# Performance work log

Hardware: AMD Instinct MI355X
Metric: run time of the kernel (lower is better)

Reference implementation:

```python
import jax, jax.numpy as jnp
import numpy as np

N_NODES = 100000
N_EDGES = 1600000
IN_F = 64
OUT_F = 64
GRID_SIZE = 5
SPLINE_ORDER = 3
GRID_MIN, GRID_MAX = -1.0, 1.0
N_COEF = GRID_SIZE + SPLINE_ORDER  # 8 spline coefficients per (in,out)


def make_grid():
    # Extended knot grid, shape (IN_F, GRID_SIZE + 2*SPLINE_ORDER + 1)
    h = (GRID_MAX - GRID_MIN) / GRID_SIZE
    pts = jnp.arange(-SPLINE_ORDER, GRID_SIZE + SPLINE_ORDER + 1, dtype=jnp.float32) * h + GRID_MIN
    return jnp.tile(pts[None, :], (IN_F, 1))


def b_splines(x, grid):
    # x: (N, IN_F) -> bases: (N, IN_F, N_COEF) via Cox-de Boor recursion
    xe = x[..., None]
    bases = ((xe >= grid[:, :-1]) & (xe < grid[:, 1:])).astype(x.dtype)
    for j in range(1, SPLINE_ORDER + 1):
        left = (xe - grid[:, : -(j + 1)]) / (grid[:, j:-1] - grid[:, : -(j + 1)])
        right = (grid[:, j + 1:] - xe) / (grid[:, j + 1:] - grid[:, 1:-j])
        bases = left * bases[..., :-1] + right * bases[..., 1:]
    return bases


def kan_apply(x, base_w, spline_w, grid):
    # base path: silu(x) @ W_b^T ; spline path: flattened B-spline bases @ W_s^T
    base = jnp.matmul(jax.nn.silu(x), base_w.T)
    sp = b_splines(x, grid).reshape(x.shape[0], -1)          # (N, IN_F*N_COEF)
    spline = jnp.matmul(sp, spline_w.reshape(OUT_F, -1).T)    # (N, OUT_F)
    return base + spline


def setup_inputs() -> dict:
    key = jax.random.key(0)
    k1, k2, k3, k4, k5, k6 = jax.random.split(key, 6)
    x = jax.random.normal(k1, (N_NODES, IN_F), dtype=jnp.float32)
    edge_index = jax.random.randint(k2, (2, N_EDGES), 0, N_NODES, dtype=jnp.int32)
    s = 1.0 / np.sqrt(IN_F)
    base_w_layer = jax.random.normal(k3, (OUT_F, IN_F), dtype=jnp.float32) * s
    spline_w_layer = jax.random.normal(k4, (OUT_F, IN_F, N_COEF), dtype=jnp.float32) * 0.1 * s
    base_w_conv = jax.random.normal(k5, (OUT_F, IN_F), dtype=jnp.float32) * s
    spline_w_conv = jax.random.normal(k6, (OUT_F, IN_F, N_COEF), dtype=jnp.float32) * 0.1 * s
    return {
        "x": x,
        "base_w_layer": base_w_layer,
        "spline_w_layer": spline_w_layer,
        "base_w_conv": base_w_conv,
        "spline_w_conv": spline_w_conv,
        "edge_index": edge_index,
    }


def reference(x, base_w_layer, spline_w_layer, base_w_conv, spline_w_conv, edge_index):
    grid = make_grid()
    src, dst = edge_index[0], edge_index[1]
    # A_hat symmetric normalization: deg^{-1/2}[src] * deg^{-1/2}[dst]
    deg = jax.ops.segment_sum(jnp.ones(src.shape[0], x.dtype), dst, num_segments=N_NODES)
    dinv = jnp.where(deg > 0, jax.lax.rsqrt(jnp.maximum(deg, 1.0)), 0.0)
    coef = dinv[src] * dinv[dst]                              # (E,)
    msg = x[src] * coef[:, None]                              # (E, IN_F) gather
    agg = jax.ops.segment_sum(msg, dst, num_segments=N_NODES) # (N, IN_F) scatter-add
    # aggregate_first=True: KAN transform applied after aggregation
    h_layer = kan_apply(x, base_w_layer, spline_w_layer, grid)
    h_conv = kan_apply(agg, base_w_conv, spline_w_conv, grid)
    return h_layer + h_conv
```

## Files before the change

### kernel.cpp

```cpp
#include <hip/hip_runtime.h>
#include <math.h>

#define N_NODES 100000
#define N_EDGES 1600000
#define IN_F 64
#define OUT_F 64

#define K_SLOT 10
#define CH_IF 16
#define AST 172
#define AGH 33
#define NB 64
#define NTHR 256
#define EMAXW 448

#define NBUCK 256
#define NBUCK_USED 196
#define BSH 9
#define BCAP 9728
#define BUCK_N 512
#define EPT 8
#define EPB 2048

#define NODES_PAD 100352
#define WF_U16 (8 * 20 * 512)
#define WG_SLOTS (WF_U16 / 2)
#define CSR_CAP (NBUCK_USED * BCAP)
#define OFF_DINV 0
#define OFF_ROWPTR (OFF_DINV + NODES_PAD)
#define OFF_ROWEND (OFF_ROWPTR + NODES_PAD)
#define OFF_WT (OFF_ROWEND + NODES_PAD)
#define OFF_BF (OFF_WT + WG_SLOTS)
#define OFF_CSR (OFF_BF + 256)
#define FIXED_SLOTS (OFF_CSR + CSR_CAP)
#define XH_SLOTS (N_NODES * IN_F / 2)
#define OFF_XH FIXED_SLOTS
#define FIXED2 (FIXED_SLOTS + XH_SLOTS)
#define AGG_ELEMS (N_NODES * IN_F)

typedef __attribute__((ext_vector_type(8))) short bf16x8;
typedef __attribute__((ext_vector_type(4))) short bf16x4;
typedef __attribute__((ext_vector_type(4))) float f32x4;

__device__ __forceinline__ unsigned int bf16_rne(float v) {
    unsigned int u = __float_as_uint(v);
    u += 0x7FFFu + ((u >> 16) & 1u);
    return u >> 16;
}

__global__ __launch_bounds__(256)
void bucket_bin_kernel(const int* __restrict__ ei, int* __restrict__ bf,
                       int2* __restrict__ pairs,
                       const float* __restrict__ x, unsigned short* __restrict__ xh) {
    __shared__ int lh[NBUCK];
    __shared__ int lbase[NBUCK];
    int t = threadIdx.x;
    lh[t] = 0;
    __syncthreads();
    int e0 = blockIdx.x * EPB;
    int d[EPT], s[EPT], lp[EPT];
#pragma unroll
    for (int k = 0; k < EPT; ++k) {
        int e = e0 + k * 256 + t;
        bool ok = e < N_EDGES;
        d[k] = ok ? ei[N_EDGES + e] : -1;
        s[k] = ok ? ei[e] : 0;
        lp[k] = ok ? atomicAdd(&lh[d[k] >> BSH], 1) : 0;
    }
    __syncthreads();
    if (lh[t]) {
        int r = atomicAdd(&bf[t], lh[t]);
        int cap = (t + 1) * BCAP - lh[t];
        lbase[t] = r > cap ? cap : r;
    }
    __syncthreads();
#pragma unroll
    for (int k = 0; k < EPT; ++k) {
        if (d[k] >= 0) {
            int b = d[k] >> BSH;
            pairs[lbase[b] + lp[k]] = make_int2(d[k], s[k]);
        }
    }
    int total = gridDim.x * 256;
    for (int i = blockIdx.x * 256 + t; i * 4 < N_NODES * IN_F; i += total) {
        float4 v = *(const float4*)&x[i * 4];
        uint2 u;
        u.x = bf16_rne(v.x) | (bf16_rne(v.y) << 16);
        u.y = bf16_rne(v.z) | (bf16_rne(v.w) << 16);
        *(uint2*)&xh[i * 4] = u;
    }
}

__global__ __launch_bounds__(BUCK_N)
void bucket_build_kernel(const int2* __restrict__ pairs, const int* __restrict__ bf,
                         int* __restrict__ rowptr, int* __restrict__ rowend,
                         float* __restrict__ dinv, int* __restrict__ csr) {
    __shared__ int ldeg[BUCK_N];
    __shared__ int sb[BUCK_N];
    __shared__ int lpos[BUCK_N];
    int t = threadIdx.x;
    int b = blockIdx.x;
    int base = b * BCAP;
    int cnt = bf[b] - base;
    if (cnt > BCAP) cnt = BCAP;
    ldeg[t] = 0;
    __syncthreads();
    for (int j = t; j < cnt; j += BUCK_N) atomicAdd(&ldeg[pairs[base + j].x & (BUCK_N - 1)], 1);
    __syncthreads();
    int v = ldeg[t];
    sb[t] = v;
    __syncthreads();
    for (int off = 1; off < BUCK_N; off <<= 1) {
        int add = (t >= off) ? sb[t - off] : 0;
        __syncthreads();
        sb[t] += add;
        __syncthreads();
    }
    int excl = sb[t] - v;
    int node = (b << BSH) + t;
    if (node < N_NODES) {
        rowptr[node] = base + excl;
        rowend[node] = base + excl + v;
        dinv[node] = (v > 0) ? rsqrtf((float)v) : 0.0f;
    }
    lpos[t] = base + excl;
    __syncthreads();
    for (int j = t; j < cnt; j += BUCK_N) {
        int2 p = pairs[base + j];
        int pos = atomicAdd(&lpos[p.x & (BUCK_N - 1)], 1);
        csr[pos] = p.y;
    }
}

__global__ __launch_bounds__(256)
void gather_kernel(const float* __restrict__ x, const int* __restrict__ csr,
                   const int* __restrict__ rowptr, const int* __restrict__ rowend,
                   const float* __restrict__ dinv, float* __restrict__ agg) {
    int wid = (int)((blockIdx.x * 256 + threadIdx.x) >> 6);
    int lane = threadIdx.x & 63;
    if (wid >= N_NODES) return;
    int start = rowptr[wid];
    int end = rowend[wid];
    float acc = 0.0f;
    int j = start;
    for (; j + 3 < end; j += 4) {
        int s0 = csr[j], s1 = csr[j + 1], s2 = csr[j + 2], s3 = csr[j + 3];
        float a0 = x[s0 * 64 + lane] * dinv[s0];
        float a1 = x[s1 * 64 + lane] * dinv[s1];
        float a2 = x[s2 * 64 + lane] * dinv[s2];
        float a3 = x[s3 * 64 + lane] * dinv[s3];
        acc += a0 + a1 + a2 + a3;
    }
    for (; j < end; ++j) {
        int s = csr[j];
        acc += x[s * 64 + lane] * dinv[s];
    }
    agg[wid * 64 + lane] = acc * dinv[wid];
}

__global__ void deg_kernel(const int* __restrict__ ei, float* __restrict__ deg) {
    int e = blockIdx.x * blockDim.x + threadIdx.x;
    if (e < N_EDGES) atomicAdd(&deg[ei[N_EDGES + e]], 1.0f);
}
__global__ void dinv_kernel(float* __restrict__ deg) {
    int n = blockIdx.x * blockDim.x + threadIdx.x;
    if (n < N_NODES) {
        float d = deg[n];
        deg[n] = (d > 0.0f) ? rsqrtf(d) : 0.0f;
    }
}
__global__ void scatter_kernel(const float* __restrict__ x, const int* __restrict__ ei,
                               const float* __restrict__ dinv, float* __restrict__ agg) {
    long long gtid = (long long)blockIdx.x * blockDim.x + threadIdx.x;
    int wid = (int)(gtid >> 6);
    int lane = threadIdx.x & 63;
    if (wid >= N_EDGES) return;
    int s = ei[wid];
    int d = ei[N_EDGES + wid];
    float c = dinv[s] * dinv[d];
    atomicAdd(&agg[d * 64 + lane], x[s * 64 + lane] * c);
}

__global__ void wprep_kernel(const float* __restrict__ bwl, const float* __restrict__ swl,
                             const float* __restrict__ bwc, const float* __restrict__ swc,
                             unsigned short* __restrict__ Wf, int* __restrict__ bf) {
    int gid = blockIdx.x * blockDim.x + threadIdx.x;
    if (bf && gid < NBUCK) bf[gid] = gid * BCAP;
    if (gid >= WF_U16) return;
    int fr = gid >> 9;
    int lj = gid & 511;
    int lane = lj >> 3, j = lj & 7;
    int ch = fr / 20, r2 = fr - ch * 20;
    int s = r2 >> 2, t = r2 & 3;
    int o = t * 16 + (lane & 15);
    int kk = ((lane >> 4) << 3) + s * 32 + j;
    int iL = kk / K_SLOT, c = kk - iL * K_SLOT;
    int i = (ch & 3) * CH_IF + iL;
    int path = ch >> 2;
    const float* bw = path ? bwc : bwl;
    const float* sw = path ? swc : swl;
    float v = 0.0f;
    if (c == 8) v = bw[o * IN_F + i];
    else if (c < 8) v = sw[o * 512 + i * 8 + c];
    Wf[gid] = (unsigned short)bf16_rne(v);
}

__device__ __forceinline__ void write_feat(unsigned short* Arow, int iL, float v) {
    unsigned int* Au = (unsigned int*)(Arow + iL * K_SLOT);
    float sig = __builtin_amdgcn_rcpf(1.0f + __expf(-v));
    Au[0] = 0u; Au[1] = 0u; Au[2] = 0u; Au[3] = 0u;
    Au[4] = bf16_rne(v * sig);
    float s5 = (v + 2.2f) * 2.5f;
    float fm = floorf(s5);
    int m = (int)fm;
    if (m >= 0 && m <= 10) {
        float t = s5 - fm;
        float omt = 1.0f - t;
        float t2 = t * t, t3 = t2 * t;
        float n0 = omt * omt * omt * (1.0f / 6.0f);
        float n3 = t3 * (1.0f / 6.0f);
        float n1 = 0.66666666f - t2 + 0.5f * t3;
        float n2 = 1.0f - n0 - n1 - n3;
        unsigned short* As = Arow + iL * K_SLOT;
        if (m >= 3)           As[m - 3] = (unsigned short)bf16_rne(n0);
        if (m >= 2 && m <= 9) As[m - 2] = (unsigned short)bf16_rne(n1);
        if (m >= 1 && m <= 8) As[m - 1] = (unsigned short)bf16_rne(n2);
        if (m <= 7)           As[m]     = (unsigned short)bf16_rne(n3);
    }
}

__global__ __launch_bounds__(NTHR, 4)
void kan_fused_kernel(const float* __restrict__ x, const unsigned short* __restrict__ xh,
                      const int* __restrict__ csr, const int* __restrict__ rowptr,
                      const int* __restrict__ rowend, const float* __restrict__ dinv,
                      const unsigned short* __restrict__ Wf, float* __restrict__ out) {
    __shared__ __align__(16) unsigned short A_lds[NB * AST];
    __shared__ unsigned int agg_lds[NB * AGH];
    __shared__ int csr_lds[4 * EMAXW];

    int tid = threadIdx.x;
    int nbase = blockIdx.x * NB;
    int wid = tid >> 6;
    int lane = tid & 63;
    int nloc0 = (wid << 4) + (lane & 15);
    int q = lane >> 4;
    int node0 = nbase + nloc0;
    bool ok0 = node0 < N_NODES;

    const float4 z4 = make_float4(0.f, 0.f, 0.f, 0.f);
    float4 vx[4];
#pragma unroll
    for (int c = 0; c < 4; ++c)
        vx[c] = ok0 ? *(const float4*)&x[node0 * 64 + c * CH_IF + q * 4] : z4;

    int wn0 = nbase + (wid << 4);
    int s0w = 0, slenw = 0;
    int* wcsr = &csr_lds[wid * EMAXW];
    if (wn0 < N_NODES) {
        int wnL = wn0 + 15;
        if (wnL >= N_NODES) wnL = N_NODES - 1;
        s0w = rowptr[wn0];
        slenw = rowend[wnL] - s0w;
        int cap = slenw < EMAXW ? slenw : EMAXW;
        for (int i = lane; i < cap; i += 64) wcsr[i] = csr[s0w + i];
    }

    f32x4 acc[4];
#pragma unroll
    for (int t = 0; t < 4; ++t) acc[t] = (f32x4){0.f, 0.f, 0.f, 0.f};

    int kfrag = (lane >> 4) * 8;
    const unsigned short* Abase = &A_lds[nloc0 * AST + kfrag];
    unsigned short* Arow = &A_lds[nloc0 * AST];
    const bf16x8* Bbase = (const bf16x8*)Wf + lane;

    auto do_chunk = [&](int chunk) {
        float vv[4];
        if (chunk < 4) {
            vv[0] = vx[chunk].x; vv[1] = vx[chunk].y; vv[2] = vx[chunk].z; vv[3] = vx[chunk].w;
        } else {
            int b2 = (chunk - 4) * 8 + q * 2;
            unsigned u0 = agg_lds[nloc0 * AGH + b2];
            unsigned u1 = agg_lds[nloc0 * AGH + b2 + 1];
            vv[0] = __uint_as_float(u0 << 16);
            vv[1] = __uint_as_float(u0 & 0xFFFF0000u);
            vv[2] = __uint_as_float(u1 << 16);
            vv[3] = __uint_as_float(u1 & 0xFFFF0000u);
        }
#pragma unroll
        for (int jj = 0; jj < 4; ++jj) write_feat(Arow, q * 4 + jj, vv[jj]);
#pragma unroll
        for (int s = 0; s < 5; ++s) {
            bf16x4 alo = *(const bf16x4*)(Abase + s * 32);
            bf16x4 ahi = *(const bf16x4*)(Abase + s * 32 + 4);
            bf16x8 a = __builtin_shufflevector(alo, ahi, 0, 1, 2, 3, 4, 5, 6, 7);
#pragma unroll
            for (int t = 0; t < 4; ++t) {
                bf16x8 b = Bbase[((chunk * 5 + s) * 4 + t) * 64];
                acc[t] = __builtin_amdgcn_mfma_f32_16x16x32_bf16(a, b, acc[t], 0, 0, 0);
            }
        }
    };

    auto do_gather = [&]() {
        int half = lane >> 5;
        int l = lane & 31;
        const unsigned int* xh32 = (const unsigned int*)xh;
        for (int p = 0; p < 8; ++p) {
            int nloc = (wid << 4) + (p << 1) + half;
            int nd = nbase + nloc;
            float ax = 0.f, ay = 0.f, dn = 0.f;
            if (nd < N_NODES) {
                dn = dinv[nd];
                int j = rowptr[nd] - s0w;
                int end = rowend[nd] - s0w;
                if (end <= EMAXW) {
                    for (; j + 15 < end; j += 16) {
                        int sa[16]; unsigned ua[16]; float da[16];
#pragma unroll
                        for (int k = 0; k < 16; ++k) sa[k] = wcsr[j + k];
#pragma unroll
                        for (int k = 0; k < 16; ++k) ua[k] = xh32[sa[k] * 32 + l];
#pragma unroll
                        for (int k = 0; k < 16; ++k) da[k] = dinv[sa[k]];
#pragma unroll
                        for (int k = 0; k < 16; ++k) {
                            ax += __uint_as_float(ua[k] << 16) * da[k];
                            ay += __uint_as_float(ua[k] & 0xFFFF0000u) * da[k];
                        }
                    }
                    for (; j + 3 < end; j += 4) {
                        int s0 = wcsr[j], s1 = wcsr[j + 1], s2 = wcsr[j + 2], s3 = wcsr[j + 3];
                        unsigned u0 = xh32[s0 * 32 + l], u1 = xh32[s1 * 32 + l];
                        unsigned u2 = xh32[s2 * 32 + l], u3 = xh32[s3 * 32 + l];
                        float d0 = dinv[s0], d1 = dinv[s1], d2 = dinv[s2], d3 = dinv[s3];
                        ax += __uint_as_float(u0 << 16) * d0 + __uint_as_float(u1 << 16) * d1
                            + __uint_as_float(u2 << 16) * d2 + __uint_as_float(u3 << 16) * d3;
                        ay += __uint_as_float(u0 & 0xFFFF0000u) * d0 + __uint_as_float(u1 & 0xFFFF0000u) * d1
                            + __uint_as_float(u2 & 0xFFFF0000u) * d2 + __uint_as_float(u3 & 0xFFFF0000u) * d3;
                    }
                    for (; j < end; ++j) {
                        int s = wcsr[j];
                        unsigned u = xh32[s * 32 + l];
                        float d = dinv[s];
                        ax += __uint_as_float(u << 16) * d;
                        ay += __uint_as_float(u & 0xFFFF0000u) * d;
                    }
                } else {
                    for (int g = rowptr[nd]; g < rowend[nd]; ++g) {
                        int s = csr[g];
                        unsigned u = xh32[s * 32 + l];
                        float d = dinv[s];
                        ax += __uint_as_float(u << 16) * d;
                        ay += __uint_as_float(u & 0xFFFF0000u) * d;
                    }
                }
            }
            agg_lds[nloc * AGH + l] = bf16_rne(ax * dn) | (bf16_rne(ay * dn) << 16);
        }
    };

    if ((blockIdx.x & 1) == 0) {
#pragma unroll
        for (int c = 0; c < 4; ++c) do_chunk(c);
        do_gather();
#pragma unroll
        for (int c = 4; c < 8; ++c) do_chunk(c);
    } else {
        do_gather();
#pragma unroll
        for (int c = 0; c < 8; ++c) do_chunk(c);
    }

#pragma unroll
    for (int t = 0; t < 4; ++t) {
#pragma unroll
        for (int r = 0; r < 4; ++r) {
            int nd = nbase + (wid << 4) + (lane >> 4) * 4 + r;
            if (nd < N_NODES) out[nd * 64 + t * 16 + (lane & 15)] = acc[t][r];
        }
    }
}

__global__ __launch_bounds__(NTHR, 8)
void kan_mfma_kernel(const float* __restrict__ x, const float* __restrict__ agg,
                     const unsigned short* __restrict__ Wf, float* __restrict__ out) {
    __shared__ __align__(16) unsigned short A_lds[NB * AST];

    int tid = threadIdx.x;
    int nbase = blockIdx.x * NB;
    int wid = tid >> 6;
    int lane = tid & 63;
    int n = tid & (NB - 1);
    int grp = wid;
    int node = nbase + n;
    bool ok = node < N_NODES;
    const float4 z4 = make_float4(0.f, 0.f, 0.f, 0.f);
    float4 vx[4], va[4];
#pragma unroll
    for (int qq = 0; qq < 4; ++qq)
        vx[qq] = ok ? *(const float4*)&x[node * 64 + qq * CH_IF + grp * 4] : z4;
#pragma unroll
    for (int qq = 0; qq < 4; ++qq)
        va[qq] = ok ? *(const float4*)&agg[node * 64 + qq * CH_IF + grp * 4] : z4;

    f32x4 acc[4];
#pragma unroll
    for (int t = 0; t < 4; ++t) acc[t] = (f32x4){0.f, 0.f, 0.f, 0.f};

    int arow = (wid << 4) + (lane & 15);
    int kfrag = (lane >> 4) * 8;
    const unsigned short* Abase = &A_lds[arow * AST + kfrag];
    const bf16x8* Bbase = (const bf16x8*)Wf + lane;

#pragma unroll
    for (int chunk = 0; chunk < 8; ++chunk) {
        const float4 v4 = (chunk < 4) ? vx[chunk] : va[chunk - 4];
        {
            float vv[4] = {v4.x, v4.y, v4.z, v4.w};
            unsigned short* Arow = &A_lds[n * AST];
#pragma unroll
            for (int jj = 0; jj < 4; ++jj) write_feat(Arow, grp * 4 + jj, vv[jj]);
        }
        __syncthreads();
        {
#pragma unroll
            for (int s = 0; s < 5; ++s) {
                bf16x4 alo = *(const bf16x4*)(Abase + s * 32);
                bf16x4 ahi = *(const bf16x4*)(Abase + s * 32 + 4);
                bf16x8 a = __builtin_shufflevector(alo, ahi, 0, 1, 2, 3, 4, 5, 6, 7);
#pragma unroll
                for (int t = 0; t < 4; ++t) {
                    bf16x8 b = Bbase[((chunk * 5 + s) * 4 + t) * 64];
                    acc[t] = __builtin_amdgcn_mfma_f32_16x16x32_bf16(a, b, acc[t], 0, 0, 0);
                }
            }
        }
        __syncthreads();
    }

#pragma unroll
    for (int t = 0; t < 4; ++t) {
#pragma unroll
        for (int r = 0; r < 4; ++r) {
            int nd = nbase + (wid << 4) + (lane >> 4) * 4 + r;
            if (nd < N_NODES) out[nd * 64 + t * 16 + (lane & 15)] = acc[t][r];
        }
    }
}

extern "C" void kernel_launch(void* const* d_in, const int* in_sizes, int n_in,
                              void* d_out, int out_size, void* d_ws, size_t ws_size,
                              hipStream_t stream) {
    const float* x   = (const float*)d_in[0];
    const float* bwl = (const float*)d_in[1];
    const float* swl = (const float*)d_in[2];
    const float* bwc = (const float*)d_in[3];
    const float* swc = (const float*)d_in[4];
    const int*   ei  = (const int*)d_in[5];
    float* out = (float*)d_out;

    float* ws = (float*)d_ws;
    float* dinv = ws + OFF_DINV;
    int* rowptr = (int*)(ws + OFF_ROWPTR);
    int* rowend = (int*)(ws + OFF_ROWEND);
    unsigned short* Wf = (unsigned short*)(ws + OFF_WT);
    int* bf = (int*)(ws + OFF_BF);
    int* csr = (int*)(ws + OFF_CSR);
    unsigned short* xh = (unsigned short*)(ws + OFF_XH);

    const bool has_csr = ws_size >= (size_t)FIXED_SLOTS * sizeof(float);
    const bool has_xh  = ws_size >= (size_t)FIXED2 * sizeof(float);
    const size_t big_base = has_xh ? (size_t)FIXED2 : (size_t)FIXED_SLOTS;
    const bool big_in_ws = ws_size >= (big_base + (size_t)AGG_ELEMS) * sizeof(float);
    float* bigbuf = (has_csr && big_in_ws) ? (ws + big_base) : out;
    int2* pairs = (int2*)bigbuf;
    float* agg = bigbuf;

    if (has_csr) {
        wprep_kernel<<<(WF_U16 + 255) / 256, 256, 0, stream>>>(bwl, swl, bwc, swc, Wf, bf);
        bucket_bin_kernel<<<(N_EDGES + EPB - 1) / EPB, 256, 0, stream>>>(ei, bf, pairs, x, xh);
        bucket_build_kernel<<<NBUCK_USED, BUCK_N, 0, stream>>>(pairs, bf, rowptr, rowend, dinv, csr);
        if (has_xh) {
            kan_fused_kernel<<<(N_NODES + NB - 1) / NB, NTHR, 0, stream>>>(
                x, xh, csr, rowptr, rowend, dinv, Wf, out);
        } else {
            gather_kernel<<<(N_NODES * 64 + 255) / 256, 256, 0, stream>>>(x, csr, rowptr, rowend, dinv, agg);
            kan_mfma_kernel<<<(N_NODES + NB - 1) / NB, NTHR, 0, stream>>>(x, agg, Wf, out);
        }
    } else {
        float* deg = dinv;
        hipMemsetAsync(deg, 0, (size_t)NODES_PAD * sizeof(float), stream);
        deg_kernel<<<(N_EDGES + 255) / 256, 256, 0, stream>>>(ei, deg);
        dinv_kernel<<<(N_NODES + 255) / 256, 256, 0, stream>>>(deg);
        hipMemsetAsync(agg, 0, (size_t)AGG_ELEMS * sizeof(float), stream);
        long long scatter_threads = (long long)N_EDGES * 64;
        int scatter_blocks = (int)((scatter_threads + 255) / 256);
        scatter_kernel<<<scatter_blocks, 256, 0, stream>>>(x, ei, deg, agg);
        wprep_kernel<<<(WF_U16 + 255) / 256, 256, 0, stream>>>(bwl, swl, bwc, swc, Wf, (int*)0);
        kan_mfma_kernel<<<(N_NODES + NB - 1) / NB, NTHR, 0, stream>>>(x, agg, Wf, out);
    }
}
```

Baseline: 157.0 us.

## Stage bucketed edge pairs in LDS and drop per-wave CSR staging in fused kernel

```diff
diff --git a/kernel.cpp b/kernel.cpp
--- a/kernel.cpp
+++ b/kernel.cpp
@@ -12,7 +12,6 @@
 #define AGH 33
 #define NB 64
 #define NTHR 256
-#define EMAXW 448
 
 #define NBUCK 256
 #define NBUCK_USED 196
@@ -53,40 +52,62 @@
                        int2* __restrict__ pairs,
                        const float* __restrict__ x, unsigned short* __restrict__ xh) {
     __shared__ int lh[NBUCK];
-    __shared__ int lbase[NBUCK];
+    __shared__ int lbs[NBUCK];
+    __shared__ int lgb[NBUCK];
+    __shared__ int2 spair[EPB];
+    __shared__ int  sdst[EPB];
     int t = threadIdx.x;
     lh[t] = 0;
     __syncthreads();
     int e0 = blockIdx.x * EPB;
+    int nE = N_EDGES - e0; if (nE > EPB) nE = EPB; if (nE < 0) nE = 0;
     int d[EPT], s[EPT], lp[EPT];
 #pragma unroll
     for (int k = 0; k < EPT; ++k) {
-        int e = e0 + k * 256 + t;
-        bool ok = e < N_EDGES;
+        int idx = k * 256 + t;
+        bool ok = idx < nE;
+        int e = e0 + idx;
         d[k] = ok ? ei[N_EDGES + e] : -1;
         s[k] = ok ? ei[e] : 0;
         lp[k] = ok ? atomicAdd(&lh[d[k] >> BSH], 1) : 0;
     }
     __syncthreads();
-    if (lh[t]) {
-        int r = atomicAdd(&bf[t], lh[t]);
-        int cap = (t + 1) * BCAP - lh[t];
-        lbase[t] = r > cap ? cap : r;
-    }
+    int v = lh[t];
+    lbs[t] = v;
+    __syncthreads();
+    for (int off = 1; off < NBUCK; off <<= 1) {
+        int add = (t >= off) ? lbs[t - off] : 0;
+        __syncthreads();
+        lbs[t] += add;
+        __syncthreads();
+    }
+    int excl = lbs[t] - v;
+    if (v) {
+        int r = atomicAdd(&bf[t], v);
+        int cap = (t + 1) * BCAP - v;
+        lgb[t] = r > cap ? cap : r;
+    }
+    __syncthreads();
+    lbs[t] = excl;
     __syncthreads();
 #pragma unroll
     for (int k = 0; k < EPT; ++k) {
         if (d[k] >= 0) {
             int b = d[k] >> BSH;
-            pairs[lbase[b] + lp[k]] = make_int2(d[k], s[k]);
-        }
-    }
+            int sp = lbs[b] + lp[k];
+            spair[sp] = make_int2(d[k], s[k]);
+            sdst[sp] = lgb[b] + lp[k];
+        }
+    }
+    __syncthreads();
+    for (int p = t; p < nE; p += 256) pairs[sdst[p]] = spair[p];
+
     int total = gridDim.x * 256;
     for (int i = blockIdx.x * 256 + t; i * 4 < N_NODES * IN_F; i += total) {
-        float4 v = *(const float4*)&x[i * 4];
+        float4 vv = *(const float4*)&x[i * 4];
         uint2 u;
-        u.x = bf16_rne(v.x) | (bf16_rne(v.y) << 16);
-        u.y = bf16_rne(v.z) | (bf16_rne(v.w) << 16);
+        u.x = bf16_rne(vv.x) | (bf16_rne(vv.y) << 16);
+        u.y = bf16_rne(vv.z) | (bf16_rne(vv.w) << 16);
         *(uint2*)&xh[i * 4] = u;
     }
 }
@@ -229,14 +250,13 @@
     }
 }
 
-__global__ __launch_bounds__(NTHR, 4)
+__global__ __launch_bounds__(NTHR, 5)
 void kan_fused_kernel(const float* __restrict__ x, const unsigned short* __restrict__ xh,
                       const int* __restrict__ csr, const int* __restrict__ rowptr,
                       const int* __restrict__ rowend, const float* __restrict__ dinv,
                       const unsigned short* __restrict__ Wf, float* __restrict__ out) {
     __shared__ __align__(16) unsigned short A_lds[NB * AST];
     __shared__ unsigned int agg_lds[NB * AGH];
-    __shared__ int csr_lds[4 * EMAXW];
 
     int tid = threadIdx.x;
     int nbase = blockIdx.x * NB;
@@ -252,18 +272,6 @@
 #pragma unroll
     for (int c = 0; c < 4; ++c)
         vx[c] = ok0 ? *(const float4*)&x[node0 * 64 + c * CH_IF + q * 4] : z4;
-
-    int wn0 = nbase + (wid << 4);
-    int s0w = 0, slenw = 0;
-    int* wcsr = &csr_lds[wid * EMAXW];
-    if (wn0 < N_NODES) {
-        int wnL = wn0 + 15;
-        if (wnL >= N_NODES) wnL = N_NODES - 1;
-        s0w = rowptr[wn0];
-        slenw = rowend[wnL] - s0w;
-        int cap = slenw < EMAXW ? slenw : EMAXW;
-        for (int i = lane; i < cap; i += 64) wcsr[i] = csr[s0w + i];
-    }
 
     f32x4 acc[4];
 #pragma unroll
@@ -312,48 +320,38 @@
             float ax = 0.f, ay = 0.f, dn = 0.f;
             if (nd < N_NODES) {
                 dn = dinv[nd];
-                int j = rowptr[nd] - s0w;
-                int end = rowend[nd] - s0w;
-                if (end <= EMAXW) {
-                    for (; j + 15 < end; j += 16) {
-                        int sa[16]; unsigned ua[16]; float da[16];
-#pragma unroll
-                        for (int k = 0; k < 16; ++k) sa[k] = wcsr[j + k];
-#pragma unroll
-                        for (int k = 0; k < 16; ++k) ua[k] = xh32[sa[k] * 32 + l];
-#pragma unroll
-                        for (int k = 0; k < 16; ++k) da[k] = dinv[sa[k]];
-#pragma unroll
-                        for (int k = 0; k < 16; ++k) {
-                            ax += __uint_as_float(ua[k] << 16) * da[k];
-                            ay += __uint_as_float(ua[k] & 0xFFFF0000u) * da[k];
-                        }
+                int j = rowptr[nd];
+                int end = rowend[nd];
+                for (; j + 15 < end; j += 16) {
+                    int sa[16]; unsigned ua[16]; float da[16];
+#pragma unroll
+                    for (int k = 0; k < 16; ++k) sa[k] = csr[j + k];
+#pragma unroll
+                    for (int k = 0; k < 16; ++k) ua[k] = xh32[sa[k] * 32 + l];
+#pragma unroll
+                    for (int k = 0; k < 16; ++k) da[k] = dinv[sa[k]];
+#pragma unroll
+                    for (int k = 0; k < 16; ++k) {
+                        ax += __uint_as_float(ua[k] << 16) * da[k];
+                        ay += __uint_as_float(ua[k] & 0xFFFF0000u) * da[k];
                     }
-                    for (; j + 3 < end; j += 4) {
-                        int s0 = wcsr[j], s1 = wcsr[j + 1], s2 = wcsr[j + 2], s3 = wcsr[j + 3];
-                        unsigned u0 = xh32[s0 * 32 + l], u1 = xh32[s1 * 32 + l];
-                        unsigned u2 = xh32[s2 * 32 + l], u3 = xh32[s3 * 32 + l];
-                        float d0 = dinv[s0], d1 = dinv[s1], d2 = dinv[s2], d3 = dinv[s3];
-                        ax += __uint_as_float(u0 << 16) * d0 + __uint_as_float(u1 << 16) * d1
-                            + __uint_as_float(u2 << 16) * d2 + __uint_as_float(u3 << 16) * d3;
-                        ay += __uint_as_float(u0 & 0xFFFF0000u) * d0 + __uint_as_float(u1 & 0xFFFF0000u) * d1
-                            + __uint_as_float(u2 & 0xFFFF0000u) * d2 + __uint_as_float(u3 & 0xFFFF0000u) * d3;
-                    }
-                    for (; j < end; ++j) {
-                        int s = wcsr[j];
-                        unsigned u = xh32[s * 32 + l];
-                        float d = dinv[s];
-                        ax += __uint_as_float(u << 16) * d;
-                        ay += __uint_as_float(u & 0xFFFF0000u) * d;
-                    }
-                } else {
-                    for (int g = rowptr[nd]; g < rowend[nd]; ++g) {
-                        int s = csr[g];
-                        unsigned u = xh32[s * 32 + l];
-                        float d = dinv[s];
-                        ax += __uint_as_float(u << 16) * d;
-                        ay += __uint_as_float(u & 0xFFFF0000u) * d;
-                    }
+                }
+                for (; j + 3 < end; j += 4) {
+                    int s0 = csr[j], s1 = csr[j + 1], s2 = csr[j + 2], s3 = csr[j + 3];
+                    unsigned u0 = xh32[s0 * 32 + l], u1 = xh32[s1 * 32 + l];
+                    unsigned u2 = xh32[s2 * 32 + l], u3 = xh32[s3 * 32 + l];
+                    float d0 = dinv[s0], d1 = dinv[s1], d2 = dinv[s2], d3 = dinv[s3];
+                    ax += __uint_as_float(u0 << 16) * d0 + __uint_as_float(u1 << 16) * d1
+                        + __uint_as_float(u2 << 16) * d2 + __uint_as_float(u3 << 16) * d3;
+                    ay += __uint_as_float(u0 & 0xFFFF0000u) * d0 + __uint_as_float(u1 & 0xFFFF0000u) * d1
+                        + __uint_as_float(u2 & 0xFFFF0000u) * d2 + __uint_as_float(u3 & 0xFFFF0000u) * d3;
+                }
+                for (; j < end; ++j) {
+                    int s = csr[j];
+                    unsigned u = xh32[s * 32 + l];
+                    float d = dinv[s];
+                    ax += __uint_as_float(u << 16) * d;
+                    ay += __uint_as_float(u & 0xFFFF0000u) * d;
                 }
             }
             agg_lds[nloc * AGH + l] = bf16_rne(ax * dn) | (bf16_rne(ay * dn) << 16);
```

New measurement: 181.4 us. +15.6%, slower.
